# Kernel tuning notes

Measured on AMD Instinct MI355X. Metric: run time of the kernel, lower is better.

Reference implementation:

```python
import jax, jax.numpy as jnp
import numpy as np

N_NODES = 50000
N_EDGES = 640000
N_REL = 200
D_IN = 128
D_OUT = 128


def setup_inputs() -> dict:
    key = jax.random.key(0)
    k1, k2, k3, k4, k5, k6 = jax.random.split(key, 6)
    x = jax.random.normal(k1, (N_NODES, D_IN), dtype=jnp.float32)
    edge_index = jax.random.randint(k2, (2, N_EDGES), 0, N_NODES, dtype=jnp.int64)
    edge_type = jax.random.randint(k3, (N_EDGES,), 0, N_REL, dtype=jnp.int64)
    rel_emb = jax.random.normal(k4, (N_REL, D_IN), dtype=jnp.float32)
    # nn.Linear weights stored as [out_features, in_features]
    W_lin = jax.random.normal(k5, (D_OUT, D_IN), dtype=jnp.float32) * (1.0 / np.sqrt(D_IN))
    # xavier_uniform for attn kernel [1, D_IN]
    limit = np.sqrt(6.0 / (1 + D_IN))
    W_attn = jax.random.uniform(k6, (1, D_IN), dtype=jnp.float32, minval=-limit, maxval=limit)
    return {"x": x, "edge_index": edge_index, "edge_type": edge_type,
            "rel_emb": rel_emb, "W_lin": W_lin, "W_attn": W_attn}


def reference(x, edge_index, edge_type, rel_emb, W_lin, W_attn):
    # x: [N, D_in]; edge_index: [2, E]; edge_type: [E]; rel_emb: [R, D_in]
    x_trans = x @ W_lin.T                       # [N, D_out]
    src_idx, tgt_idx = edge_index[0], edge_index[1]
    h_src = x[src_idx]                          # [E, D_in] gather
    h_rel = rel_emb[edge_type]                  # [E, D_in] gather
    sum_feat = h_src + h_rel                    # [E, D_in]
    attn = jax.nn.sigmoid(sum_feat @ W_attn.T)  # [E, 1]
    msg = x_trans[src_idx] * attn               # [E, D_out]
    out = jax.ops.segment_sum(msg, tgt_idx, num_segments=x.shape[0])  # [N, D_out]
    return jax.nn.relu(out)
```

## Files before the change

### kernel.cpp

```cpp
#include <hip/hip_runtime.h>
#include <hip/hip_bf16.h>

#define N_NODES 50000
#define N_EDGES 640000
#define N_REL   200
#define D       128
#define CAP     64
#define RANGES  8
#define NODES_PER_RANGE (N_NODES / RANGES)
#define CHUNK_EDGES 2560
#define N_CHUNKS (N_EDGES / CHUNK_EDGES)

typedef __attribute__((ext_vector_type(8))) short short8;
typedef __attribute__((ext_vector_type(4))) float floatx4;

__device__ __forceinline__ unsigned short f2bf(float f) {
    unsigned u = __float_as_uint(f);
    u += 0x7FFF + ((u >> 16) & 1);
    return (unsigned short)(u >> 16);
}

__device__ __forceinline__ float sigmoidf(float x) {
    return 1.f / (1.f + __expf(-x));
}

__global__ void setup_kernel(const float* __restrict__ W,
                             const float* __restrict__ x,
                             const float* __restrict__ rel,
                             const float* __restrict__ Wattn,
                             unsigned short* __restrict__ Wbf,
                             float* __restrict__ s_rel,
                             float* __restrict__ s_node,
                             int* __restrict__ count) {
    const int b = blockIdx.x;
    if (b < 64) {
        const int i = b * 256 + threadIdx.x;
        Wbf[i] = f2bf(W[i]);
    } else if (b < 114) {
        const int wave = (b - 64) * 4 + (threadIdx.x >> 6);
        const int lane = threadIdx.x & 63;
        if (wave < N_REL) {
            const float* __restrict__ row = rel + (size_t)wave * D;
            float a = fmaf(row[lane], Wattn[lane],
                           row[lane + 64] * Wattn[lane + 64]);
#pragma unroll
            for (int off = 32; off; off >>= 1)
                a += __shfl_down(a, off);
            if (lane == 0) s_rel[wave] = a;
        }
    } else if (b < 310) {
        const int i = (b - 114) * 256 + threadIdx.x;
        if (i < N_NODES) count[i] = 0;
    } else {
        const int node = (b - 310) * 8 + (threadIdx.x >> 5);
        const int sub  = threadIdx.x & 31;
        if (node < N_NODES) {
            const float4 xv = ((const float4*)(x + (size_t)node * D))[sub];
            const float4 wv = ((const float4*)Wattn)[sub];
            float a = xv.x * wv.x + xv.y * wv.y + xv.z * wv.z + xv.w * wv.w;
#pragma unroll
            for (int off = 16; off; off >>= 1)
                a += __shfl_xor(a, off);
            if (sub == 0) s_node[node] = a;
        }
    }
}

__global__ void xtrans_mfma_kernel(const float* __restrict__ x,
                                   const unsigned short* __restrict__ Wbf,
                                   unsigned short* __restrict__ xt) {
    const int wid = (blockIdx.x * blockDim.x + threadIdx.x) >> 6;
    if (wid >= N_NODES / 16) return;
    const int lane = threadIdx.x & 63;
    const int r16  = lane & 15;
    const int quad = lane >> 4;
    const int m0   = wid * 16;

    short8 af[4];
#pragma unroll
    for (int s = 0; s < 4; ++s) {
        const int k0 = s * 32 + quad * 8;
        const float* __restrict__ xr = x + (size_t)(m0 + r16) * D + k0;
        const float4 lo = *(const float4*)(xr);
        const float4 hi = *(const float4*)(xr + 4);
        short8 a;
        a[0] = (short)f2bf(lo.x); a[1] = (short)f2bf(lo.y);
        a[2] = (short)f2bf(lo.z); a[3] = (short)f2bf(lo.w);
        a[4] = (short)f2bf(hi.x); a[5] = (short)f2bf(hi.y);
        a[6] = (short)f2bf(hi.z); a[7] = (short)f2bf(hi.w);
        af[s] = a;
    }

#pragma unroll
    for (int t = 0; t < 8; ++t) {
        floatx4 acc = {0.f, 0.f, 0.f, 0.f};
#pragma unroll
        for (int s = 0; s < 4; ++s) {
            const int k0 = s * 32 + quad * 8;
            const short8 b = *(const short8*)(Wbf + (size_t)(t * 16 + r16) * D + k0);
            acc = __builtin_amdgcn_mfma_f32_16x16x32_bf16(af[s], b, acc, 0, 0, 0);
        }
#pragma unroll
        for (int r = 0; r < 4; ++r) {
            const int orow = m0 + quad * 4 + r;
            xt[(size_t)orow * D + t * 16 + r16] = f2bf(acc[r]);
        }
    }
}

__global__ void scatter_kernel(const int* __restrict__ src_idx,
                               const int* __restrict__ tgt_idx,
                               const int* __restrict__ etype,
                               const float* __restrict__ s_node,
                               const float* __restrict__ s_rel,
                               int* __restrict__ count,
                               unsigned* __restrict__ sorted) {
    const int b     = blockIdx.x;
    const int lo    = (b & 7) * NODES_PER_RANGE;
    const int hi    = lo + NODES_PER_RANGE;
    const int base  = (b >> 3) * CHUNK_EDGES + threadIdx.x;

#pragma unroll
    for (int it = 0; it < CHUNK_EDGES / 256; ++it) {
        const int e = base + it * 256;
        const int t = tgt_idx[e];
        if (t >= lo && t < hi) {
            const int s = src_idx[e];
            const int r = etype[e];
            const float logit = s_node[s] + s_rel[r];
            const unsigned rec =
                ((unsigned)f2bf(sigmoidf(logit)) << 16) | (unsigned)s;
            const int k = atomicAdd(&count[t], 1);
            sorted[t * CAP + k] = rec;
        }
    }
}

__device__ __forceinline__ void gproc(unsigned r, const unsigned short* __restrict__ xt,
                                      int sub, float4& acc) {
    const unsigned src = r & 0xFFFFu;
    const float a = __uint_as_float(r & 0xFFFF0000u);
    const uint2 p = *(const uint2*)(xt + (size_t)src * D + sub * 4);
    acc.x = fmaf(a, __uint_as_float(p.x << 16),        acc.x);
    acc.y = fmaf(a, __uint_as_float(p.x & 0xFFFF0000u), acc.y);
    acc.z = fmaf(a, __uint_as_float(p.y << 16),        acc.z);
    acc.w = fmaf(a, __uint_as_float(p.y & 0xFFFF0000u), acc.w);
}

__global__ void gather_kernel(const int* __restrict__ count,
                              const unsigned* __restrict__ sorted,
                              const unsigned short* __restrict__ xt,
                              float* __restrict__ out) {
    const int wid  = (blockIdx.x * blockDim.x + threadIdx.x) >> 6;
    const int lane = threadIdx.x & 63;
    const int half = lane >> 5;
    const int sub  = lane & 31;
    const int t    = wid * 2 + half;
    if (t >= N_NODES) return;

    const int cnt = count[t];
    const unsigned* __restrict__ rec = sorted + (size_t)t * CAP;

    float4 acc = {0.f, 0.f, 0.f, 0.f};
    int i = 0;
    for (; i + 4 <= cnt; i += 4) {
        const uint4 r4 = *(const uint4*)(rec + i);
        gproc(r4.x, xt, sub, acc);
        gproc(r4.y, xt, sub, acc);
        gproc(r4.z, xt, sub, acc);
        gproc(r4.w, xt, sub, acc);
    }
    for (; i < cnt; ++i)
        gproc(rec[i], xt, sub, acc);

    float4 o;
    o.x = fmaxf(acc.x, 0.f);
    o.y = fmaxf(acc.y, 0.f);
    o.z = fmaxf(acc.z, 0.f);
    o.w = fmaxf(acc.w, 0.f);
    ((float4*)(out + (size_t)t * D))[sub] = o;
}

extern "C" void kernel_launch(void* const* d_in, const int* in_sizes, int n_in,
                              void* d_out, int out_size, void* d_ws, size_t ws_size,
                              hipStream_t stream) {
    const float* x        = (const float*)d_in[0];
    const int*   edge_idx = (const int*)d_in[1];
    const int*   etype    = (const int*)d_in[2];
    const float* rel_emb  = (const float*)d_in[3];
    const float* W_lin    = (const float*)d_in[4];
    const float* W_attn   = (const float*)d_in[5];
    float* out = (float*)d_out;

    const int* src_idx = edge_idx;
    const int* tgt_idx = edge_idx + N_EDGES;

    unsigned short* xt   = (unsigned short*)d_ws;
    float* s_node        = (float*)(xt + (size_t)N_NODES * D);
    float* s_rel         = s_node + N_NODES;
    unsigned short* Wbf  = (unsigned short*)(s_rel + N_REL);
    int*   count         = (int*)(Wbf + D * D);
    unsigned* sorted     = (unsigned*)(count + N_NODES);

    setup_kernel<<<dim3(310 + (N_NODES + 7) / 8), dim3(256), 0, stream>>>(
        W_lin, x, rel_emb, W_attn, Wbf, s_rel, s_node, count);

    xtrans_mfma_kernel<<<dim3((N_NODES / 16 * 64 + 255) / 256), dim3(256), 0, stream>>>(
        x, Wbf, xt);

    scatter_kernel<<<dim3(N_CHUNKS * RANGES), dim3(256), 0, stream>>>(
        src_idx, tgt_idx, etype, s_node, s_rel, count, sorted);

    gather_kernel<<<dim3(N_NODES / 8), dim3(256), 0, stream>>>(
        count, sorted, xt, out);
}
```

Baseline: 169.2 us.

## Bind scatter node ranges to XCDs via work-stealing cursors; widen gather loads

The scatter kernel reads the hardware XCC id and has each block pull edge chunks from a per-range atomic cursor, starting with the node range matching its XCD. The aim is for each range's atomics and record writes to stay mostly in one XCD's L2 instead of bouncing across dies. Blocks then steal chunks from other ranges once their own is exhausted. The gather kernel now gives 16 lanes to each node with 16-byte loads of 8 bf16 values, so a wave covers four nodes. The costs are an extra atomic plus two barriers per chunk, and reliance on there being 8 XCDs.

After: 361.5 us. 114% more time.

```diff
diff --git a/kernel.cpp b/kernel.cpp
--- a/kernel.cpp
+++ b/kernel.cpp
@@ -14,6 +14,8 @@
 typedef __attribute__((ext_vector_type(8))) short short8;
 typedef __attribute__((ext_vector_type(4))) float floatx4;
 
+#define HWREG_XCC_ID (20 | (0 << 6) | (31 << 11))
+
 __device__ __forceinline__ unsigned short f2bf(float f) {
     unsigned u = __float_as_uint(f);
     u += 0x7FFF + ((u >> 16) & 1);
@@ -23,6 +25,9 @@
 __device__ __forceinline__ float sigmoidf(float x) {
     return 1.f / (1.f + __expf(-x));
 }
+
+__device__ __forceinline__ float bflo(unsigned u) { return __uint_as_float(u << 16); }
+__device__ __forceinline__ float bfhi(unsigned u) { return __uint_as_float(u & 0xFFFF0000u); }
 
 __global__ void setup_kernel(const float* __restrict__ W,
                              const float* __restrict__ x,
@@ -50,7 +55,7 @@
         }
     } else if (b < 310) {
         const int i = (b - 114) * 256 + threadIdx.x;
-        if (i < N_NODES) count[i] = 0;
+        if (i < N_NODES + RANGES) count[i] = 0;
     } else {
         const int node = (b - 310) * 8 + (threadIdx.x >> 5);
         const int sub  = threadIdx.x & 31;
@@ -114,37 +119,57 @@
                                const float* __restrict__ s_node,
                                const float* __restrict__ s_rel,
                                int* __restrict__ count,
+                               int* __restrict__ cursor,
                                unsigned* __restrict__ sorted) {
-    const int b     = blockIdx.x;
-    const int lo    = (b & 7) * NODES_PER_RANGE;
-    const int hi    = lo + NODES_PER_RANGE;
-    const int base  = (b >> 3) * CHUNK_EDGES + threadIdx.x;
-
-#pragma unroll
-    for (int it = 0; it < CHUNK_EDGES / 256; ++it) {
-        const int e = base + it * 256;
-        const int t = tgt_idx[e];
-        if (t >= lo && t < hi) {
-            const int s = src_idx[e];
-            const int r = etype[e];
-            const float logit = s_node[s] + s_rel[r];
-            const unsigned rec =
-                ((unsigned)f2bf(sigmoidf(logit)) << 16) | (unsigned)s;
-            const int k = atomicAdd(&count[t], 1);
-            sorted[t * CAP + k] = rec;
-        }
-    }
-}
-
-__device__ __forceinline__ void gproc(unsigned r, const unsigned short* __restrict__ xt,
-                                      int sub, float4& acc) {
+    __shared__ int sh_chunk;
+    const unsigned my_xcd =
+        __builtin_amdgcn_s_getreg(HWREG_XCC_ID) & (RANGES - 1);
+
+    for (int j = 0; j < RANGES; ++j) {
+        const int q  = (my_xcd + j) & (RANGES - 1);
+        const int lo = q * NODES_PER_RANGE;
+        const int hi = lo + NODES_PER_RANGE;
+        for (;;) {
+            if (threadIdx.x == 0)
+                sh_chunk = atomicAdd(&cursor[q], 1);
+            __syncthreads();
+            const int c = sh_chunk;
+            __syncthreads();
+            if (c >= N_CHUNKS) break;
+
+            const int base = c * CHUNK_EDGES + threadIdx.x;
+#pragma unroll
+            for (int it = 0; it < CHUNK_EDGES / 256; ++it) {
+                const int e = base + it * 256;
+                const int t = tgt_idx[e];
+                if (t >= lo && t < hi) {
+                    const int s = src_idx[e];
+                    const int r = etype[e];
+                    const float logit = s_node[s] + s_rel[r];
+                    const unsigned rec =
+                        ((unsigned)f2bf(sigmoidf(logit)) << 16) | (unsigned)s;
+                    const int k = atomicAdd(&count[t], 1);
+                    sorted[t * CAP + k] = rec;
+                }
+            }
+        }
+    }
+}
+
+__device__ __forceinline__ void gproc8(unsigned r,
+                                       const unsigned short* __restrict__ xt,
+                                       int sub, float* acc) {
     const unsigned src = r & 0xFFFFu;
     const float a = __uint_as_float(r & 0xFFFF0000u);
-    const uint2 p = *(const uint2*)(xt + (size_t)src * D + sub * 4);
-    acc.x = fmaf(a, __uint_as_float(p.x << 16),        acc.x);
-    acc.y = fmaf(a, __uint_as_float(p.x & 0xFFFF0000u), acc.y);
-    acc.z = fmaf(a, __uint_as_float(p.y << 16),        acc.z);
-    acc.w = fmaf(a, __uint_as_float(p.y & 0xFFFF0000u), acc.w);
+    const uint4 p = *(const uint4*)(xt + (size_t)src * D + sub * 8);
+    acc[0] = fmaf(a, bflo(p.x), acc[0]);
+    acc[1] = fmaf(a, bfhi(p.x), acc[1]);
+    acc[2] = fmaf(a, bflo(p.y), acc[2]);
+    acc[3] = fmaf(a, bfhi(p.y), acc[3]);
+    acc[4] = fmaf(a, bflo(p.z), acc[4]);
+    acc[5] = fmaf(a, bfhi(p.z), acc[5]);
+    acc[6] = fmaf(a, bflo(p.w), acc[6]);
+    acc[7] = fmaf(a, bfhi(p.w), acc[7]);
 }
 
 __global__ void gather_kernel(const int* __restrict__ count,
@@ -153,32 +178,34 @@
                               float* __restrict__ out) {
     const int wid  = (blockIdx.x * blockDim.x + threadIdx.x) >> 6;
     const int lane = threadIdx.x & 63;
-    const int half = lane >> 5;
-    const int sub  = lane & 31;
-    const int t    = wid * 2 + half;
+    const int grp  = lane >> 4;
+    const int sub  = lane & 15;
+    const int t    = wid * 4 + grp;
     if (t >= N_NODES) return;
 
     const int cnt = count[t];
     const unsigned* __restrict__ rec = sorted + (size_t)t * CAP;
 
-    float4 acc = {0.f, 0.f, 0.f, 0.f};
+    float acc[8] = {0.f, 0.f, 0.f, 0.f, 0.f, 0.f, 0.f, 0.f};
     int i = 0;
     for (; i + 4 <= cnt; i += 4) {
         const uint4 r4 = *(const uint4*)(rec + i);
-        gproc(r4.x, xt, sub, acc);
-        gproc(r4.y, xt, sub, acc);
-        gproc(r4.z, xt, sub, acc);
-        gproc(r4.w, xt, sub, acc);
+        gproc8(r4.x, xt, sub, acc);
+        gproc8(r4.y, xt, sub, acc);
+        gproc8(r4.z, xt, sub, acc);
+        gproc8(r4.w, xt, sub, acc);
     }
     for (; i < cnt; ++i)
-        gproc(rec[i], xt, sub, acc);
-
-    float4 o;
-    o.x = fmaxf(acc.x, 0.f);
-    o.y = fmaxf(acc.y, 0.f);
-    o.z = fmaxf(acc.z, 0.f);
-    o.w = fmaxf(acc.w, 0.f);
-    ((float4*)(out + (size_t)t * D))[sub] = o;
+        gproc8(rec[i], xt, sub, acc);
+
+    float4 o0, o1;
+    o0.x = fmaxf(acc[0], 0.f); o0.y = fmaxf(acc[1], 0.f);
+    o0.z = fmaxf(acc[2], 0.f); o0.w = fmaxf(acc[3], 0.f);
+    o1.x = fmaxf(acc[4], 0.f); o1.y = fmaxf(acc[5], 0.f);
+    o1.z = fmaxf(acc[6], 0.f); o1.w = fmaxf(acc[7], 0.f);
+    float* orow = out + (size_t)t * D + sub * 8;
+    *(float4*)(orow)     = o0;
+    *(float4*)(orow + 4) = o1;
 }
 
 extern "C" void kernel_launch(void* const* d_in, const int* in_sizes, int n_in,
@@ -200,7 +227,8 @@
     float* s_rel         = s_node + N_NODES;
     unsigned short* Wbf  = (unsigned short*)(s_rel + N_REL);
     int*   count         = (int*)(Wbf + D * D);
-    unsigned* sorted     = (unsigned*)(count + N_NODES);
+    int*   cursor        = count + N_NODES;
+    unsigned* sorted     = (unsigned*)(count + N_NODES + RANGES);
 
     setup_kernel<<<dim3(310 + (N_NODES + 7) / 8), dim3(256), 0, stream>>>(
         W_lin, x, rel_emb, W_attn, Wbf, s_rel, s_node, count);
@@ -209,8 +237,8 @@
         x, Wbf, xt);
 
     scatter_kernel<<<dim3(N_CHUNKS * RANGES), dim3(256), 0, stream>>>(
-        src_idx, tgt_idx, etype, s_node, s_rel, count, sorted);
-
-    gather_kernel<<<dim3(N_NODES / 8), dim3(256), 0, stream>>>(
+        src_idx, tgt_idx, etype, s_node, s_rel, count, cursor, sorted);
+
+    gather_kernel<<<dim3((N_NODES + 15) / 16), dim3(256), 0, stream>>>(
         count, sorted, xt, out);
 }
```
